# Kernel optimization log

Measured on AMD Instinct MI355X. Metric: run time of the kernel, lower is better.

The kernel has to match this reference:

```python
import jax, jax.numpy as jnp
import numpy as np

GF = 25  # gauss_filter_dim

def _gauss(std):
    n = np.arange(GF) - (GF - 1) / 2.0
    return np.exp(-0.5 * (n / std) ** 2).astype(np.float32)

def _ln(x, g, b, eps=1e-5):
    m = jnp.mean(x, -1, keepdims=True)
    v = jnp.mean((x - m) ** 2, -1, keepdims=True)
    return (x - m) * jax.lax.rsqrt(v + eps) * g + b

def _prelu(x, a):
    return jnp.where(x >= 0, x, a * x)

def _lrelu(x, s):
    return jnp.where(x >= 0, x, s * x)

B, D, H, NB = 32768, 128, 256, 4
C = 32  # 2**5

def setup_inputs() -> dict:
    key = jax.random.key(0)
    ks = jax.random.split(key, 16)
    rn = lambda k, s, sc=0.05: (jax.random.normal(k, s, dtype=jnp.float32) * sc)
    filters = jnp.asarray(np.stack([_gauss(0.5), _gauss(1.0), _gauss(3.0)]))  # [3,25]
    return {
        'x': jax.random.normal(ks[0], (B, D), dtype=jnp.float32),
        'filters': filters,
        'W1': rn(ks[1], (H, D)), 'b1': jnp.zeros((H,), jnp.float32),
        'a0': jnp.float32(0.25),  # PReLU scalar
        'g0': jnp.ones((H,), jnp.float32), 'be0': jnp.zeros((H,), jnp.float32),
        'Wc1': rn(ks[2], (NB, C, H)), 'bc1': jnp.zeros((NB, C), jnp.float32),
        'Wc2': rn(ks[3], (NB, C, H)), 'bc2': jnp.zeros((NB, C), jnp.float32),
        'Wc3': rn(ks[4], (NB, C, H)), 'bc3': jnp.zeros((NB, C), jnp.float32),
        'Wcat': rn(ks[5], (NB, H, 3 * C)), 'bcat': jnp.zeros((NB, H), jnp.float32),
        'g1': jnp.ones((NB, H), jnp.float32), 'be1': jnp.zeros((NB, H), jnp.float32),
        'Wf1': rn(ks[6], (NB, H, H)), 'bf1': jnp.zeros((NB, H), jnp.float32),
        'af': jnp.full((NB,), 0.25, jnp.float32),
        'Wf2': rn(ks[7], (NB, H, H)), 'bf2': jnp.zeros((NB, H), jnp.float32),
        'g2': jnp.ones((NB, H), jnp.float32), 'be2': jnp.zeros((NB, H), jnp.float32),
        'Wout': rn(ks[8], (1, H)), 'bout': jnp.zeros((1,), jnp.float32),
    }

def reference(x, filters, W1, b1, a0, g0, be0, Wc1, bc1, Wc2, bc2, Wc3, bc3,
              Wcat, bcat, g1, be1, Wf1, bf1, af, Wf2, bf2, g2, be2, Wout, bout):
    out = _prelu(x @ W1.T + b1, a0)
    out = _ln(out, g0, be0)
    kern = filters[:, None, :]  # [3, 1, GF] -> 3 output channels, 1 input channel
    nb = Wc1.shape[0]
    for i in range(nb):
        res = out
        # batched 'same' 1D conv with the three Gaussian filters in one call: [B,3,H]
        conv = jax.lax.conv_general_dilated(out[:, None, :], kern, (1,), 'SAME')
        x1 = _lrelu(conv[:, 0] @ Wc1[i].T + bc1[i], 0.1)
        x2 = _lrelu(conv[:, 1] @ Wc2[i].T + bc2[i], 0.1)
        x3 = _lrelu(conv[:, 2] @ Wc3[i].T + bc3[i], 0.1)
        out = jnp.concatenate([x1, x2, x3], axis=1) @ Wcat[i].T + bcat[i]
        out = _ln(out + res, g1[i], be1[i])
        res = out
        h = _prelu(out @ Wf1[i].T + bf1[i], af[i])  # dropout inactive (eval)
        h = h @ Wf2[i].T + bf2[i]
        out = _ln(h + res, g2[i], be2[i])
    return out @ Wout.T + bout
```

## Files before the change

### kernel.cpp

```cpp
#include <hip/hip_runtime.h>

typedef __attribute__((ext_vector_type(8))) short bf16x8;
typedef __attribute__((ext_vector_type(4))) float f32x4;

__device__ __forceinline__ float bf2f(unsigned short u) {
    union { unsigned u; float f; } x; x.u = (unsigned)u << 16; return x.f;
}
__device__ __forceinline__ unsigned short f2bf(float f) {
    union { float f; unsigned u; } x; x.f = f;
    unsigned r = x.u + 0x7fffu + ((x.u >> 16) & 1u);
    return (unsigned short)(r >> 16);
}

#define GLDS(src, dst) __builtin_amdgcn_global_load_lds( \
    (const __attribute__((address_space(1))) void*)(src), \
    (__attribute__((address_space(3))) void*)(dst), 16, 0, 0)

__global__ __launch_bounds__(256) void prep(
    const float* __restrict__ filters,
    const float* __restrict__ Wc1, const float* __restrict__ Wc2, const float* __restrict__ Wc3,
    const float* __restrict__ bc1, const float* __restrict__ bc2, const float* __restrict__ bc3,
    const float* __restrict__ W1, const float* __restrict__ Wcat,
    const float* __restrict__ Wf1, const float* __restrict__ Wf2,
    unsigned short* __restrict__ W1b, unsigned short* __restrict__ wceffb,
    float* __restrict__ bceff, unsigned short* __restrict__ Wcatb,
    unsigned short* __restrict__ Wf1b, unsigned short* __restrict__ Wf2b)
{
    int idx = blockIdx.x * 256 + threadIdx.x;
    if (idx < 65536) {
        int n = idx >> 8, k = idx & 255;
        W1b[idx] = (k < 128) ? f2bf(W1[n * 128 + k]) : (unsigned short)0;
    } else if (idx < 196608) {
        int j = idx - 65536;
        int i = j >> 15, n = (j >> 8) & 127, h = j & 255;
        if (n < 96) {
            int c = n >> 5, jj = n & 31;
            const float* Wc = (c == 0) ? Wc1 : (c == 1) ? Wc2 : Wc3;
            const float* f  = filters + c * 25;
            float acc = 0.f;
            #pragma unroll
            for (int k = 0; k < 25; ++k) {
                int hh = h + 12 - k;
                if (hh >= 0 && hh < 256) acc += f[k] * Wc[(i * 32 + jj) * 256 + hh];
            }
            wceffb[j] = f2bf(acc);
            if (h == 0) {
                const float* bc = (c == 0) ? bc1 : (c == 1) ? bc2 : bc3;
                bceff[i * 128 + n] = bc[i * 32 + jj];
            }
        } else {
            wceffb[j] = 0;
            if (h == 0) bceff[i * 128 + n] = 0.f;
        }
    } else if (idx < 458752) {
        int j = idx - 196608;
        int i = j >> 16, rem = j & 65535, n = rem >> 8, k = rem & 255;
        Wcatb[j] = (k < 96) ? f2bf(Wcat[(i * 256 + n) * 96 + k]) : (unsigned short)0;
    } else if (idx < 720896) {
        int j = idx - 458752;
        Wf1b[j] = f2bf(Wf1[j]);
    } else if (idx < 983040) {
        int j = idx - 720896;
        Wf2b[j] = f2bf(Wf2[j]);
    }
}

template<int NKC, int NWT>
__device__ __forceinline__ void gemm_stage(
    const unsigned short* __restrict__ Wg,
    const float* __restrict__ bias,
    const unsigned short* actIn, unsigned short* actOut,
    unsigned short* wlds,
    int actmode, const float* alphap,
    const unsigned short* resbuf,
    const float* g, const float* be,
    int finaldot, const float* Wout, const float* boutp, float* outg, int rowbase)
{
    constexpr int NT = NWT * 4;
    const int tid  = threadIdx.x;
    const int lane = tid & 63;
    const int wave = tid >> 6;
    const int wm   = wave >> 2;
    const int wn   = wave & 3;
    const int l15  = lane & 15;
    const int hi   = lane >> 4;

    f32x4 acc[4][NWT];
    #pragma unroll
    for (int mt = 0; mt < 4; ++mt)
        #pragma unroll
        for (int nt = 0; nt < NWT; ++nt) acc[mt][nt] = (f32x4){0.f, 0.f, 0.f, 0.f};

    #pragma unroll
    for (int tt = 0; tt < NT / 8; ++tt) {
        const int t = wave + tt * 8;
        GLDS(Wg + (t * 16 + l15) * 256 + hi * 8, wlds + t * 512);
    }
    __syncthreads();

    for (int kc = 0; kc < NKC; ++kc) {
        const int cur = (kc & 1) * 8192;
        if (kc + 1 < NKC) {
            const int nxt = ((kc + 1) & 1) * 8192;
            #pragma unroll
            for (int tt = 0; tt < NT / 8; ++tt) {
                const int t = wave + tt * 8;
                GLDS(Wg + (t * 16 + l15) * 256 + (kc + 1) * 32 + hi * 8,
                     wlds + nxt + t * 512);
            }
        }
        bf16x8 bfr[4], afr[NWT];
        #pragma unroll
        for (int mt = 0; mt < 4; ++mt)
            bfr[mt] = *(const bf16x8*)(actIn + ((wm * 4 + mt) * 8 + kc) * 512 + lane * 8);
        #pragma unroll
        for (int nt = 0; nt < NWT; ++nt)
            afr[nt] = *(const bf16x8*)(wlds + cur + (wn * NWT + nt) * 512 + lane * 8);
        #pragma unroll
        for (int mt = 0; mt < 4; ++mt)
            #pragma unroll
            for (int nt = 0; nt < NWT; ++nt)
                acc[mt][nt] = __builtin_amdgcn_mfma_f32_16x16x32_bf16(
                    afr[nt], bfr[mt], acc[mt][nt], 0, 0, 0);
        __syncthreads();
    }

    const float alpha = alphap ? alphap[0] : 0.1f;
    float vv[4][NWT][4];
    #pragma unroll
    for (int mt = 0; mt < 4; ++mt) {
        #pragma unroll
        for (int nt = 0; nt < NWT; ++nt) {
            const int nb = wn * (NWT * 16) + nt * 16 + hi * 4;
            const float4 bs = *(const float4*)(bias + nb);
            float t0 = acc[mt][nt][0] + bs.x;
            float t1 = acc[mt][nt][1] + bs.y;
            float t2 = acc[mt][nt][2] + bs.z;
            float t3 = acc[mt][nt][3] + bs.w;
            if (actmode) {
                t0 = t0 >= 0.f ? t0 : alpha * t0;
                t1 = t1 >= 0.f ? t1 : alpha * t1;
                t2 = t2 >= 0.f ? t2 : alpha * t2;
                t3 = t3 >= 0.f ? t3 : alpha * t3;
            }
            if (resbuf) {
                const int ro = ((wm * 4 + mt) * 8 + (nb >> 5)) * 512
                             + (l15 + ((nb >> 3) & 3) * 16) * 8 + (nb & 7);
                const ushort4 rv = *(const ushort4*)(resbuf + ro);
                t0 += bf2f(rv.x); t1 += bf2f(rv.y); t2 += bf2f(rv.z); t3 += bf2f(rv.w);
            }
            vv[mt][nt][0] = t0; vv[mt][nt][1] = t1;
            vv[mt][nt][2] = t2; vv[mt][nt][3] = t3;
        }
    }

    float* lnred = (float*)wlds;
    float mean[4], rstd[4];
    if (g) {
        #pragma unroll
        for (int mt = 0; mt < 4; ++mt) {
            float s = 0.f, q = 0.f;
            #pragma unroll
            for (int nt = 0; nt < NWT; ++nt)
                #pragma unroll
                for (int r = 0; r < 4; ++r) { const float v = vv[mt][nt][r]; s += v; q += v * v; }
            s += __shfl_xor(s, 16); s += __shfl_xor(s, 32);
            q += __shfl_xor(q, 16); q += __shfl_xor(q, 32);
            if (hi == 0)
                *(float2*)(lnred + (wm * 64 + mt * 16 + l15) * 8 + wn * 2) = make_float2(s, q);
        }
        __syncthreads();
        #pragma unroll
        for (int mt = 0; mt < 4; ++mt) {
            const int m = wm * 64 + mt * 16 + l15;
            const float4 p0 = *(const float4*)(lnred + m * 8);
            const float4 p1 = *(const float4*)(lnred + m * 8 + 4);
            const float s = p0.x + p0.z + p1.x + p1.z;
            const float q = p0.y + p0.w + p1.y + p1.w;
            const float mu = s * (1.f / 256.f);
            mean[mt] = mu;
            rstd[mt] = rsqrtf(q * (1.f / 256.f) - mu * mu + 1e-5f);
        }
    }

    float* dotp = (float*)wlds + 2048;
    #pragma unroll
    for (int mt = 0; mt < 4; ++mt) {
        float dp = 0.f;
        #pragma unroll
        for (int nt = 0; nt < NWT; ++nt) {
            const int nb = wn * (NWT * 16) + nt * 16 + hi * 4;
            float o0 = vv[mt][nt][0], o1 = vv[mt][nt][1], o2 = vv[mt][nt][2], o3 = vv[mt][nt][3];
            if (g) {
                const float4 gv = *(const float4*)(g + nb);
                const float4 bv = *(const float4*)(be + nb);
                o0 = (o0 - mean[mt]) * rstd[mt] * gv.x + bv.x;
                o1 = (o1 - mean[mt]) * rstd[mt] * gv.y + bv.y;
                o2 = (o2 - mean[mt]) * rstd[mt] * gv.z + bv.z;
                o3 = (o3 - mean[mt]) * rstd[mt] * gv.w + bv.w;
            }
            if (!finaldot) {
                const ushort4 ov = {f2bf(o0), f2bf(o1), f2bf(o2), f2bf(o3)};
                *(ushort4*)(actOut + ((wm * 4 + mt) * 8 + (nb >> 5)) * 512
                            + (l15 + ((nb >> 3) & 3) * 16) * 8 + (nb & 7)) = ov;
            } else {
                const float4 wv = *(const float4*)(Wout + nb);
                dp += o0 * wv.x + o1 * wv.y + o2 * wv.z + o3 * wv.w;
            }
        }
        if (finaldot) {
            dp += __shfl_xor(dp, 16); dp += __shfl_xor(dp, 32);
            if (hi == 0) dotp[(wm * 64 + mt * 16 + l15) * 4 + wn] = dp;
        }
    }
    if (finaldot) {
        __syncthreads();
        if (tid < 128) {
            const float4 pp = *(const float4*)(dotp + tid * 4);
            outg[rowbase + tid] = pp.x + pp.y + pp.z + pp.w + boutp[0];
        }
    }
    __syncthreads();
}

__global__ __launch_bounds__(512, 2) void mega(
    const float* __restrict__ x,
    const unsigned short* __restrict__ W1b, const float* __restrict__ b1,
    const float* __restrict__ a0, const float* __restrict__ g0, const float* __restrict__ be0,
    const unsigned short* __restrict__ wceffb, const float* __restrict__ bceff,
    const unsigned short* __restrict__ Wcatb, const float* __restrict__ bcat,
    const float* __restrict__ g1, const float* __restrict__ be1,
    const unsigned short* __restrict__ Wf1b, const float* __restrict__ bf1,
    const float* __restrict__ af,
    const unsigned short* __restrict__ Wf2b, const float* __restrict__ bf2,
    const float* __restrict__ g2, const float* __restrict__ be2,
    const float* __restrict__ Wout, const float* __restrict__ boutp,
    float* __restrict__ outg)
{
    __shared__ __align__(16) unsigned short actA[32768];
    __shared__ __align__(16) unsigned short actB[32768];
    __shared__ __align__(16) unsigned short wlds[16384];

    const int tid = threadIdx.x;
    const int rowbase = blockIdx.x * 128;

    {
        const int r = tid >> 2, q = tid & 3;
        const float* xp = x + (size_t)(rowbase + r) * 128 + q * 32;
        #pragma unroll
        for (int gi = 0; gi < 8; ++gi) {
            const float4 xv = *(const float4*)(xp + gi * 4);
            const int j = q * 32 + gi * 4;
            const ushort4 o = {f2bf(xv.x), f2bf(xv.y), f2bf(xv.z), f2bf(xv.w)};
            *(ushort4*)(actB + ((r >> 4) * 8 + (j >> 5)) * 512
                        + ((r & 15) + ((j >> 3) & 3) * 16) * 8 + (j & 7)) = o;
        }
        __syncthreads();
    }

    gemm_stage<4, 4>(W1b, b1, actB, actA, wlds, 1, a0, nullptr, g0, be0,
                     0, nullptr, nullptr, nullptr, 0);

    for (int it = 0; it < 4; ++it) {
        gemm_stage<8, 2>(wceffb + it * 32768, bceff + it * 128, actA, actB, wlds,
                         2, nullptr, nullptr, nullptr, nullptr, 0, nullptr, nullptr, nullptr, 0);
        gemm_stage<4, 4>(Wcatb + it * 65536, bcat + it * 256, actB, actA, wlds,
                         0, nullptr, actA, g1 + it * 256, be1 + it * 256,
                         0, nullptr, nullptr, nullptr, 0);
        gemm_stage<8, 4>(Wf1b + it * 65536, bf1 + it * 256, actA, actB, wlds,
                         1, af + it, nullptr, nullptr, nullptr, 0, nullptr, nullptr, nullptr, 0);
        gemm_stage<8, 4>(Wf2b + it * 65536, bf2 + it * 256, actB, actA, wlds,
                         0, nullptr, actA, g2 + it * 256, be2 + it * 256,
                         (it == 3) ? 1 : 0, Wout, boutp, outg, rowbase);
    }
}

extern "C" void kernel_launch(void* const* d_in, const int* in_sizes, int n_in,
                              void* d_out, int out_size, void* d_ws, size_t ws_size,
                              hipStream_t stream)
{
    const float* x       = (const float*)d_in[0];
    const float* filters = (const float*)d_in[1];
    const float* W1      = (const float*)d_in[2];
    const float* b1      = (const float*)d_in[3];
    const float* a0      = (const float*)d_in[4];
    const float* g0      = (const float*)d_in[5];
    const float* be0     = (const float*)d_in[6];
    const float* Wc1     = (const float*)d_in[7];
    const float* bc1     = (const float*)d_in[8];
    const float* Wc2     = (const float*)d_in[9];
    const float* bc2     = (const float*)d_in[10];
    const float* Wc3     = (const float*)d_in[11];
    const float* bc3     = (const float*)d_in[12];
    const float* Wcat    = (const float*)d_in[13];
    const float* bcat    = (const float*)d_in[14];
    const float* g1      = (const float*)d_in[15];
    const float* be1     = (const float*)d_in[16];
    const float* Wf1     = (const float*)d_in[17];
    const float* bf1     = (const float*)d_in[18];
    const float* af      = (const float*)d_in[19];
    const float* Wf2     = (const float*)d_in[20];
    const float* bf2     = (const float*)d_in[21];
    const float* g2      = (const float*)d_in[22];
    const float* be2     = (const float*)d_in[23];
    const float* Wout    = (const float*)d_in[24];
    const float* boutp   = (const float*)d_in[25];
    float* outf = (float*)d_out;

    unsigned short* p = (unsigned short*)d_ws;
    unsigned short* W1b    = p;
    unsigned short* wceffb = p + 65536;
    unsigned short* Wcatb  = p + 196608;
    unsigned short* Wf1b   = p + 458752;
    unsigned short* Wf2b   = p + 720896;
    float*          bceff  = (float*)(p + 983040);

    prep<<<dim3(3840), dim3(256), 0, stream>>>(
        filters, Wc1, Wc2, Wc3, bc1, bc2, bc3, W1, Wcat, Wf1, Wf2,
        W1b, wceffb, bceff, Wcatb, Wf1b, Wf2b);

    mega<<<dim3(256), dim3(512), 0, stream>>>(
        x, W1b, b1, a0, g0, be0, wceffb, bceff, Wcatb, bcat, g1, be1,
        Wf1b, bf1, af, Wf2b, bf2, g2, be2, Wout, boutp, outf);
}
```

Baseline: 141.7 us.

## Load weight fragments straight from global into registers, dropping LDS staging

New measurement: 158.1 us. 11.6% more time.

```diff
diff --git a/kernel.cpp b/kernel.cpp
--- a/kernel.cpp
+++ b/kernel.cpp
@@ -11,10 +11,6 @@
     unsigned r = x.u + 0x7fffu + ((x.u >> 16) & 1u);
     return (unsigned short)(r >> 16);
 }
-
-#define GLDS(src, dst) __builtin_amdgcn_global_load_lds( \
-    (const __attribute__((address_space(1))) void*)(src), \
-    (__attribute__((address_space(3))) void*)(dst), 16, 0, 0)
 
 __global__ __launch_bounds__(256) void prep(
     const float* __restrict__ filters,
@@ -70,13 +66,12 @@
     const unsigned short* __restrict__ Wg,
     const float* __restrict__ bias,
     const unsigned short* actIn, unsigned short* actOut,
-    unsigned short* wlds,
+    float* scratch,
     int actmode, const float* alphap,
     const unsigned short* resbuf,
     const float* g, const float* be,
     int finaldot, const float* Wout, const float* boutp, float* outg, int rowbase)
 {
-    constexpr int NT = NWT * 4;
     const int tid  = threadIdx.x;
     const int lane = tid & 63;
     const int wave = tid >> 6;
@@ -91,39 +86,37 @@
         #pragma unroll
         for (int nt = 0; nt < NWT; ++nt) acc[mt][nt] = (f32x4){0.f, 0.f, 0.f, 0.f};
 
+    const unsigned short* wbase = Wg + ((size_t)(wn * NWT) * 16 + l15) * 256 + hi * 8;
+    const unsigned short* abase = actIn + (wm * 4) * 8 * 512 + lane * 8;
+
+    bf16x8 w0[NWT], w1[NWT], a0[4], a1[4];
+
+    #define LOADW(dst, kc) { _Pragma("unroll") \
+        for (int nt = 0; nt < NWT; ++nt) \
+            dst[nt] = *(const bf16x8*)(wbase + nt * 16 * 256 + (kc) * 32); }
+    #define LOADA(dst, kc) { _Pragma("unroll") \
+        for (int mt = 0; mt < 4; ++mt) \
+            dst[mt] = *(const bf16x8*)(abase + (mt * 8 + (kc)) * 512); }
+    #define FMAS(areg, wreg) { \
+        __builtin_amdgcn_s_setprio(1); \
+        _Pragma("unroll") \
+        for (int mt = 0; mt < 4; ++mt) { _Pragma("unroll") \
+            for (int nt = 0; nt < NWT; ++nt) \
+                acc[mt][nt] = __builtin_amdgcn_mfma_f32_16x16x32_bf16( \
+                    wreg[nt], areg[mt], acc[mt][nt], 0, 0, 0); } \
+        __builtin_amdgcn_s_setprio(0); }
+
+    LOADW(w0, 0); LOADA(a0, 0);
     #pragma unroll
-    for (int tt = 0; tt < NT / 8; ++tt) {
-        const int t = wave + tt * 8;
-        GLDS(Wg + (t * 16 + l15) * 256 + hi * 8, wlds + t * 512);
-    }
-    __syncthreads();
-
-    for (int kc = 0; kc < NKC; ++kc) {
-        const int cur = (kc & 1) * 8192;
-        if (kc + 1 < NKC) {
-            const int nxt = ((kc + 1) & 1) * 8192;
-            #pragma unroll
-            for (int tt = 0; tt < NT / 8; ++tt) {
-                const int t = wave + tt * 8;
-                GLDS(Wg + (t * 16 + l15) * 256 + (kc + 1) * 32 + hi * 8,
-                     wlds + nxt + t * 512);
-            }
-        }
-        bf16x8 bfr[4], afr[NWT];
-        #pragma unroll
-        for (int mt = 0; mt < 4; ++mt)
-            bfr[mt] = *(const bf16x8*)(actIn + ((wm * 4 + mt) * 8 + kc) * 512 + lane * 8);
-        #pragma unroll
-        for (int nt = 0; nt < NWT; ++nt)
-            afr[nt] = *(const bf16x8*)(wlds + cur + (wn * NWT + nt) * 512 + lane * 8);
-        #pragma unroll
-        for (int mt = 0; mt < 4; ++mt)
-            #pragma unroll
-            for (int nt = 0; nt < NWT; ++nt)
-                acc[mt][nt] = __builtin_amdgcn_mfma_f32_16x16x32_bf16(
-                    afr[nt], bfr[mt], acc[mt][nt], 0, 0, 0);
-        __syncthreads();
-    }
+    for (int kc = 0; kc < NKC; kc += 2) {
+        if (kc + 1 < NKC) { LOADW(w1, kc + 1); LOADA(a1, kc + 1); }
+        FMAS(a0, w0);
+        if (kc + 2 < NKC) { LOADW(w0, kc + 2); LOADA(a0, kc + 2); }
+        if (kc + 1 < NKC) FMAS(a1, w1);
+    }
+    #undef LOADW
+    #undef LOADA
+    #undef FMAS
 
     const float alpha = alphap ? alphap[0] : 0.1f;
     float vv[4][NWT][4];
@@ -154,7 +147,7 @@
         }
     }
 
-    float* lnred = (float*)wlds;
+    float* lnred = scratch;
     float mean[4], rstd[4];
     if (g) {
         #pragma unroll
@@ -183,7 +176,7 @@
         }
     }
 
-    float* dotp = (float*)wlds + 2048;
+    float* dotp = scratch + 1024;
     #pragma unroll
     for (int mt = 0; mt < 4; ++mt) {
         float dp = 0.f;
@@ -239,7 +232,7 @@
 {
     __shared__ __align__(16) unsigned short actA[32768];
     __shared__ __align__(16) unsigned short actB[32768];
-    __shared__ __align__(16) unsigned short wlds[16384];
+    __shared__ __align__(16) float scratch[1536];
 
     const int tid = threadIdx.x;
     const int rowbase = blockIdx.x * 128;
@@ -258,18 +251,20 @@
         __syncthreads();
     }
 
-    gemm_stage<4, 4>(W1b, b1, actB, actA, wlds, 1, a0, nullptr, g0, be0,
+    gemm_stage<4, 4>(W1b, b1, actB, actA, scratch, 1, a0, nullptr, g0, be0,
                      0, nullptr, nullptr, nullptr, 0);
 
     for (int it = 0; it < 4; ++it) {
-        gemm_stage<8, 2>(wceffb + it * 32768, bceff + it * 128, actA, actB, wlds,
-                         2, nullptr, nullptr, nullptr, nullptr, 0, nullptr, nullptr, nullptr, 0);
-        gemm_stage<4, 4>(Wcatb + it * 65536, bcat + it * 256, actB, actA, wlds,
+        gemm_stage<8, 2>(wceffb + it * 32768, bceff + it * 128, actA, actB, scratch,
+                         2, nullptr, nullptr, nullptr, nullptr,
+                         0, nullptr, nullptr, nullptr, 0);
+        gemm_stage<4, 4>(Wcatb + it * 65536, bcat + it * 256, actB, actA, scratch,
                          0, nullptr, actA, g1 + it * 256, be1 + it * 256,
                          0, nullptr, nullptr, nullptr, 0);
-        gemm_stage<8, 4>(Wf1b + it * 65536, bf1 + it * 256, actA, actB, wlds,
-                         1, af + it, nullptr, nullptr, nullptr, 0, nullptr, nullptr, nullptr, 0);
-        gemm_stage<8, 4>(Wf2b + it * 65536, bf2 + it * 256, actB, actA, wlds,
+        gemm_stage<8, 4>(Wf1b + it * 65536, bf1 + it * 256, actA, actB, scratch,
+                         1, af + it, nullptr, nullptr, nullptr,
+                         0, nullptr, nullptr, nullptr, 0);
+        gemm_stage<8, 4>(Wf2b + it * 65536, bf2 + it * 256, actB, actA, scratch,
                          0, nullptr, actA, g2 + it * 256, be2 + it * 256,
                          (it == 3) ? 1 : 0, Wout, boutp, outg, rowbase);
     }
```
